# Kernel tuning notes

Hardware: AMD Instinct MI355X
Metric: run time of the kernel (lower is better)

Reference implementation:

```python
import jax, jax.numpy as jnp
import numpy as np

B, D, O = 256, 4096, 16384


def setup_inputs() -> dict:
    key = jax.random.key(0)
    k1, k2, k3, k4 = jax.random.split(key, 4)
    x1 = jax.random.normal(k1, (B, D), dtype=jnp.float32)
    x2 = jax.random.normal(k2, (B, D), dtype=jnp.float32)
    # random hash buckets in [0, O) and random +/-1 signs (homogeneous: shared by both inputs)
    h1 = jax.random.randint(k3, (D,), 0, O, dtype=jnp.int32)
    s1 = jnp.where(jax.random.uniform(k4, (D,)) < 0.5, -1.0, 1.0).astype(jnp.float32)
    return {"x1": x1, "x2": x2, "h1": h1, "s1": s1, "output_size": O}


def reference(x1, x2, h1, s1, output_size):
    # psi(): count-sketch via sign-multiply + scatter-add along feature axis
    batch = x1.shape[0]
    y1 = jnp.zeros((batch, output_size), x1.dtype).at[:, h1].add(s1 * x1)  # [B, O]
    y2 = jnp.zeros((batch, output_size), x2.dtype).at[:, h1].add(s1 * x2)  # [B, O]
    # conv(): circular convolution of the two sketches via FFT pointwise product
    out = jnp.fft.ifft(jnp.fft.fft(y1, axis=-1) * jnp.fft.fft(y2, axis=-1), axis=-1)
    return out.real.astype(x1.dtype)
```

## Files before the change

### kernel.cpp

```cpp
#include <hip/hip_runtime.h>


typedef float v2 __attribute__((ext_vector_type(2)));

#define N1      8192
#define BLOCK   1024
#define DIM     4096
#define PI_F    3.14159265358979323846f
#define RS2     0.70710678118654752f
#define SLOT(e) ((e) ^ (((e) >> 4) & 15))
#define REV13(x) ((int)(__brev((unsigned)(x)) >> 19))
#define WAVE_FENCE() __asm__ volatile("s_waitcnt lgkmcnt(0)" ::: "memory")

static __device__ __forceinline__ v2 cmul(v2 a, v2 b) {
    return a.xx * b + (v2){-a.y, a.y} * b.yx;
}
static __device__ __forceinline__ v2 csqr(v2 a) { return cmul(a, a); }
static __device__ __forceinline__ v2 expi(float phi) {
    float s, c; __sincosf(phi, &s, &c); return (v2){c, s};
}

static __device__ __forceinline__ void fft8_dif(v2* r, float phi) {
    v2 W2 = expi(phi), W1 = csqr(W2), W0 = csqr(W1);
    v2 W[3] = {W0, W1, W2};
    #pragma unroll
    for (int p = 2; p >= 0; --p) {
        #pragma unroll
        for (int h = 0; h < 4; ++h) {
            const int jp = h & ((1 << p) - 1);
            const int j  = ((h >> p) << (p + 1)) | jp;
            const int ci = jp << (2 - p);
            v2 Wp = W[p], T;
            if (ci == 0)      T = Wp;
            else if (ci == 2) T = (v2){Wp.y, -Wp.x};
            else if (ci == 1) T = cmul(Wp, (v2){RS2, -RS2});
            else              T = cmul(Wp, (v2){-RS2, -RS2});
            v2 a = r[j], bb = r[j + (1 << p)];
            r[j] = a + bb;
            r[j + (1 << p)] = cmul(a - bb, T);
        }
    }
}

static __device__ __forceinline__ void fft8_dit(v2* r, float phi) {
    v2 W2 = expi(phi), W1 = csqr(W2), W0 = csqr(W1);
    v2 W[3] = {W0, W1, W2};
    #pragma unroll
    for (int p = 0; p <= 2; ++p) {
        #pragma unroll
        for (int h = 0; h < 4; ++h) {
            const int jp = h & ((1 << p) - 1);
            const int j  = ((h >> p) << (p + 1)) | jp;
            const int ci = jp << (2 - p);
            v2 Wp = W[p], T;
            if (ci == 0)      T = Wp;
            else if (ci == 2) T = (v2){-Wp.y, Wp.x};
            else if (ci == 1) T = cmul(Wp, (v2){RS2, RS2});
            else              T = cmul(Wp, (v2){-RS2, RS2});
            v2 a = r[j], bb = cmul(r[j + (1 << p)], T);
            r[j]            = a + bb;
            r[j + (1 << p)] = a - bb;
        }
    }
}

static __device__ __forceinline__ void fft8_dit0(v2* r) {
    #pragma unroll
    for (int p = 0; p <= 2; ++p) {
        #pragma unroll
        for (int h = 0; h < 4; ++h) {
            const int jp = h & ((1 << p) - 1);
            const int j  = ((h >> p) << (p + 1)) | jp;
            const int ci = jp << (2 - p);
            v2 x = r[j + (1 << p)], bb;
            if (ci == 0)      bb = x;
            else if (ci == 2) bb = (v2){-x.y, x.x};
            else if (ci == 1) bb = cmul(x, (v2){RS2, RS2});
            else              bb = cmul(x, (v2){-RS2, RS2});
            v2 a = r[j];
            r[j] = a + bb; r[j + (1 << p)] = a - bb;
        }
    }
}

static __device__ __forceinline__ void fft4_difW4(v2& r0, v2& r1, v2& r2, v2& r3, v2 W1) {
    v2 W0 = csqr(W1);
    v2 a, bb;
    a = r0; bb = r2; r0 = a + bb; r2 = cmul(a - bb, W1);
    a = r1; bb = r3; r1 = a + bb;
    { v2 d = a - bb; r3 = cmul(d, (v2){W1.y, -W1.x}); }
    a = r0; bb = r1; r0 = a + bb; r1 = cmul(a - bb, W0);
    a = r2; bb = r3; r2 = a + bb; r3 = cmul(a - bb, W0);
}
static __device__ __forceinline__ void fft4_dif04(v2& r0, v2& r1, v2& r2, v2& r3) {
    v2 a, bb;
    a = r0; bb = r2; r0 = a + bb; r2 = a - bb;
    a = r1; bb = r3; r1 = a + bb;
    { v2 d = a - bb; r3 = (v2){d.y, -d.x}; }
    a = r0; bb = r1; r0 = a + bb; r1 = a - bb;
    a = r2; bb = r3; r2 = a + bb; r3 = a - bb;
}

static __device__ __forceinline__ void pair_slot(v2* zz, int j) {
    const int k  = REV13(j);
    const int kp = (N1 - k) & (N1 - 1);
    const int j2 = REV13(kp);
    v2 A = zz[SLOT(j)], B = zz[SLOT(j2)];
    v2 C = zz[N1 + SLOT(j)], D = zz[N1 + SLOT(j2)];
    v2 E  = (v2){0.5f * (A.x + B.x),  0.5f * (A.y - B.y)};
    v2 O  = (v2){0.5f * (A.y + B.y), -0.5f * (A.x - B.x)};
    v2 F  = (v2){0.5f * (C.x + D.x),  0.5f * (C.y - D.y)};
    v2 Ov = (v2){0.5f * (C.y + D.y), -0.5f * (C.x - D.x)};
    v2 Tm = expi(-PI_F * (float)k * (1.f / 8192.f));
    v2 u = cmul(Tm, O), v = cmul(Tm, Ov);
    v2 G = cmul(E + u, F + v);
    v2 H = cmul(E - u, F - v);
    v2 S  = (v2){0.5f * (G.x + H.x), 0.5f * (G.y + H.y)};
    v2 gh = G - H;
    v2 t2 = cmul((v2){Tm.x, -Tm.y}, gh);
    v2 Dv = (v2){-0.5f * t2.y, 0.5f * t2.x};
    zz[SLOT(j)]  = S + Dv;
    zz[SLOT(j2)] = (v2){S.x - Dv.x, -(S.y - Dv.y)};
}

__launch_bounds__(BLOCK, 4)
__global__ void cbp_fft_kernel(const float* __restrict__ x1,
                               const float* __restrict__ x2,
                               const int* __restrict__ h1,
                               const float* __restrict__ s1,
                               float* __restrict__ out) {
    __shared__ v2 zz[2 * N1];
    const int tid = threadIdx.x;
    const int l   = tid & 63;
    const int b   = blockIdx.x;
    float* zf = (float*)zz;

    const float* x1r = x1 + (size_t)b * DIM;
    const float* x2r = x2 + (size_t)b * DIM;
    float sv[DIM / BLOCK], a1[DIM / BLOCK], a2[DIM / BLOCK];
    int   hv[DIM / BLOCK];
    #pragma unroll
    for (int i = 0; i < DIM / BLOCK; ++i) {
        int d = tid + (i << 10);
        sv[i] = s1[d];
        hv[i] = h1[d];
        a1[i] = x1r[d];
        a2[i] = x2r[d];
    }

    {
        float4* z4 = (float4*)zz;
        #pragma unroll
        for (int j = 0; j < 8; ++j) z4[tid + (j << 10)] = make_float4(0.f, 0.f, 0.f, 0.f);
    }
    __syncthreads();

    #pragma unroll
    for (int i = 0; i < DIM / BLOCK; ++i) {
        int  h  = hv[i];
        int  fi = (SLOT(h >> 1) << 1) | (h & 1);
        atomicAdd(&zf[fi], sv[i] * a1[i]);
        atomicAdd(&zf[2 * N1 + fi], sv[i] * a2[i]);
    }
    __syncthreads();

    const int half = tid >> 9;
    const int tt   = tid & 511;
    const int hw   = tt >> 6;
    v2* Ah = zz + half * N1;

    #pragma unroll 1
    for (int q = 0; q < 2; ++q) {
        int k  = tt + (q << 9);
        int bs = k ^ ((k >> 4) & 15);
        v2 r[8];
        #pragma unroll
        for (int j = 0; j < 8; ++j) r[j] = Ah[bs + (j << 10)];
        fft8_dif(r, (float)k * (-PI_F / 4096.f));
        #pragma unroll
        for (int j = 0; j < 8; ++j) Ah[bs + (j << 10)] = r[j];
    }
    __syncthreads();

    #pragma unroll 1
    for (int q = 0; q < 2; ++q) {
        int kk = (tt & 63) + (q << 6);
        int bE = ((hw << 10) + kk) ^ (kk >> 4);
        int bO = bE ^ 8;
        v2 r[8];
        #pragma unroll
        for (int j = 0; j < 8; ++j) r[j] = Ah[((j & 1) ? bO : bE) + (j << 7)];
        fft8_dif(r, (float)kk * (-PI_F / 512.f));
        #pragma unroll
        for (int j = 0; j < 8; ++j) Ah[((j & 1) ? bO : bE) + (j << 7)] = r[j];
    }
    WAVE_FENCE();

    #pragma unroll 1
    for (int q = 0; q < 2; ++q) {
        int g  = (hw << 3) + ((l >> 4) << 1) + q;
        int kf = l & 15;
        int a0 = (g << 7) + (kf ^ (q << 3));
        v2 r[8];
        #pragma unroll
        for (int j = 0; j < 8; ++j) r[j] = Ah[(a0 ^ j) + (j << 4)];
        fft8_dif(r, (float)kf * (-PI_F / 64.f));
        #pragma unroll
        for (int j = 0; j < 8; ++j) Ah[(a0 ^ j) + (j << 4)] = r[j];
    }
    WAVE_FENCE();

    {
        const int span  = (hw << 6) + (l & 15) + ((l >> 4) << 4);
        const int sbase = (span << 4) + (span & 15);
        v2 R[16];
        #pragma unroll
        for (int m = 0; m < 16; ++m) R[m] = Ah[sbase ^ m];
        #pragma unroll
        for (int k4 = 0; k4 < 4; ++k4) {
            float c = (k4 & 1) ? ((k4 & 2) ? 0.38268343f : 0.92387953f)
                               : ((k4 & 2) ? 0.70710678f : 1.f);
            float s = (k4 & 1) ? ((k4 & 2) ? -0.92387953f : -0.38268343f)
                               : ((k4 & 2) ? -0.70710678f : 0.f);
            fft4_difW4(R[k4], R[k4 + 4], R[k4 + 8], R[k4 + 12], (v2){c, s});
        }
        #pragma unroll
        for (int q = 0; q < 4; ++q)
            fft4_dif04(R[4 * q], R[4 * q + 1], R[4 * q + 2], R[4 * q + 3]);
        #pragma unroll
        for (int m = 0; m < 16; ++m) Ah[sbase ^ m] = R[m];
    }
    __syncthreads();

    #pragma unroll 2
    for (int i = 0; i < 4; ++i) pair_slot(zz, (tid + (i << 10)) << 1);
    if (tid == 0) pair_slot(zz, 1);
    __syncthreads();

    {
        int B1 = (tid << 3) ^ ((tid >> 1) & 15);
        v2 r[8];
        #pragma unroll
        for (int i = 0; i < 8; ++i) r[i] = zz[B1 ^ i];
        fft8_dit0(r);
        #pragma unroll
        for (int i = 0; i < 8; ++i) zz[B1 ^ i] = r[i];
    }
    WAVE_FENCE();
    {
        int g = tid >> 3, k = tid & 7;
        int base = (g << 6) + k;
        v2 r[8];
        #pragma unroll
        for (int j = 0; j < 8; ++j) r[j] = zz[SLOT(base + (j << 3))];
        fft8_dit(r, (float)k * (PI_F / 32.f));
        #pragma unroll
        for (int j = 0; j < 8; ++j) zz[SLOT(base + (j << 3))] = r[j];
    }
    WAVE_FENCE();
    {
        int k = tid & 63;
        int base0 = ((tid >> 6) << 9) + (k & ~15);
        int Kh = k >> 4, K15 = k & 15;
        int B0  = base0 + (K15 ^ Kh);
        int Bm1 = base0 + (K15 ^ (Kh + 4));
        int Bm2 = base0 + (K15 ^ (Kh + 8));
        int Bm3 = base0 + (K15 ^ (Kh + 12));
        v2 r[8];
        r[0] = zz[B0];        r[1] = zz[Bm1 + 64];
        r[2] = zz[Bm2 + 128]; r[3] = zz[Bm3 + 192];
        r[4] = zz[B0 + 256];  r[5] = zz[Bm1 + 320];
        r[6] = zz[Bm2 + 384]; r[7] = zz[Bm3 + 448];
        fft8_dit(r, (float)k * (PI_F / 256.f));
        zz[B0]        = r[0]; zz[Bm1 + 64]  = r[1];
        zz[Bm2 + 128] = r[2]; zz[Bm3 + 192] = r[3];
        zz[B0 + 256]  = r[4]; zz[Bm1 + 320] = r[5];
        zz[Bm2 + 384] = r[6]; zz[Bm3 + 448] = r[7];
    }
    __syncthreads();
    {
        int g = tid >> 9, k = tid & 511;
        int bp = ((g << 12) + k) ^ ((k >> 4) & 15);
        v2 r[8];
        #pragma unroll
        for (int j = 0; j < 8; ++j) r[j] = zz[bp + (j << 9)];
        fft8_dit(r, (float)k * (PI_F / 2048.f));
        #pragma unroll
        for (int j = 0; j < 8; ++j) zz[bp + (j << 9)] = r[j];
    }
    __syncthreads();

    {
        float* outr = out + (size_t)b * (2 * N1);
        const float inv_n1 = 1.0f / (float)N1;
        const int b5 = (tid << 2) ^ ((tid >> 2) & 15);
        v2 Tn = expi(PI_F * (float)(tid << 2) * (1.f / 4096.f));
        const v2 STEP = (v2){0.99999970586288f, 7.6699031874270e-4f};
        v2 lo[4], hi[4];
        #pragma unroll
        for (int d5 = 0; d5 < 4; ++d5) {
            v2 a  = zz[b5 ^ d5];
            v2 bb = zz[(b5 ^ d5) + 4096];
            v2 tb = cmul(Tn, bb);
            lo[d5] = a + tb;
            hi[d5] = a - tb;
            if (d5 < 3) Tn = cmul(Tn, STEP);
        }
        float4 vlo0 = make_float4(lo[0].x * inv_n1, lo[0].y * inv_n1,
                                  lo[1].x * inv_n1, lo[1].y * inv_n1);
        float4 vlo1 = make_float4(lo[2].x * inv_n1, lo[2].y * inv_n1,
                                  lo[3].x * inv_n1, lo[3].y * inv_n1);
        float4 vhi0 = make_float4(hi[0].x * inv_n1, hi[0].y * inv_n1,
                                  hi[1].x * inv_n1, hi[1].y * inv_n1);
        float4 vhi1 = make_float4(hi[2].x * inv_n1, hi[2].y * inv_n1,
                                  hi[3].x * inv_n1, hi[3].y * inv_n1);
        *(float4*)(outr + (tid << 3))          = vlo0;
        *(float4*)(outr + (tid << 3) + 4)      = vlo1;
        *(float4*)(outr + N1 + (tid << 3))     = vhi0;
        *(float4*)(outr + N1 + (tid << 3) + 4) = vhi1;
    }
}

extern "C" void kernel_launch(void* const* d_in, const int* in_sizes, int n_in,
                              void* d_out, int out_size, void* d_ws, size_t ws_size,
                              hipStream_t stream) {
    const float* x1 = (const float*)d_in[0];
    const float* x2 = (const float*)d_in[1];
    const int*   h1 = (const int*)d_in[2];
    const float* s1 = (const float*)d_in[3];
    float* out = (float*)d_out;
    const int B = in_sizes[0] / DIM;
    cbp_fft_kernel<<<B, BLOCK, 0, stream>>>(x1, x2, h1, s1, out);
}
```

Baseline: 92.10 us.

## Replace four radix-8 inverse FFT passes with three radix-16 passes

```diff
diff --git a/kernel.cpp b/kernel.cpp
--- a/kernel.cpp
+++ b/kernel.cpp
@@ -8,6 +8,8 @@
 #define DIM     4096
 #define PI_F    3.14159265358979323846f
 #define RS2     0.70710678118654752f
+#define C8      0.92387953251128675f
+#define S8      0.38268343236508977f
 #define SLOT(e) ((e) ^ (((e) >> 4) & 15))
 #define REV13(x) ((int)(__brev((unsigned)(x)) >> 19))
 #define WAVE_FENCE() __asm__ volatile("s_waitcnt lgkmcnt(0)" ::: "memory")
@@ -42,21 +44,25 @@
     }
 }
 
-static __device__ __forceinline__ void fft8_dit(v2* r, float phi) {
-    v2 W2 = expi(phi), W1 = csqr(W2), W0 = csqr(W1);
-    v2 W[3] = {W0, W1, W2};
-    #pragma unroll
-    for (int p = 0; p <= 2; ++p) {
-        #pragma unroll
-        for (int h = 0; h < 4; ++h) {
+static __device__ __forceinline__ void fft16_dit(v2* r, float phi) {
+    v2 W3 = expi(phi), W2 = csqr(W3), W1 = csqr(W2), W0 = csqr(W1);
+    v2 W[4] = {W0, W1, W2, W3};
+    #pragma unroll
+    for (int p = 0; p <= 3; ++p) {
+        #pragma unroll
+        for (int h = 0; h < 8; ++h) {
             const int jp = h & ((1 << p) - 1);
             const int j  = ((h >> p) << (p + 1)) | jp;
-            const int ci = jp << (2 - p);
+            const int ci = jp << (3 - p);
             v2 Wp = W[p], T;
             if (ci == 0)      T = Wp;
-            else if (ci == 2) T = (v2){-Wp.y, Wp.x};
-            else if (ci == 1) T = cmul(Wp, (v2){RS2, RS2});
-            else              T = cmul(Wp, (v2){-RS2, RS2});
+            else if (ci == 4) T = (v2){-Wp.y, Wp.x};
+            else if (ci == 2) T = cmul(Wp, (v2){RS2, RS2});
+            else if (ci == 6) T = cmul(Wp, (v2){-RS2, RS2});
+            else if (ci == 1) T = cmul(Wp, (v2){C8, S8});
+            else if (ci == 3) T = cmul(Wp, (v2){S8, C8});
+            else if (ci == 5) T = cmul(Wp, (v2){-S8, C8});
+            else              T = cmul(Wp, (v2){-C8, S8});
             v2 a = r[j], bb = cmul(r[j + (1 << p)], T);
             r[j]            = a + bb;
             r[j + (1 << p)] = a - bb;
@@ -64,19 +70,23 @@
     }
 }
 
-static __device__ __forceinline__ void fft8_dit0(v2* r) {
-    #pragma unroll
-    for (int p = 0; p <= 2; ++p) {
-        #pragma unroll
-        for (int h = 0; h < 4; ++h) {
+static __device__ __forceinline__ void fft16_dit0(v2* r) {
+    #pragma unroll
+    for (int p = 0; p <= 3; ++p) {
+        #pragma unroll
+        for (int h = 0; h < 8; ++h) {
             const int jp = h & ((1 << p) - 1);
             const int j  = ((h >> p) << (p + 1)) | jp;
-            const int ci = jp << (2 - p);
+            const int ci = jp << (3 - p);
             v2 x = r[j + (1 << p)], bb;
             if (ci == 0)      bb = x;
-            else if (ci == 2) bb = (v2){-x.y, x.x};
-            else if (ci == 1) bb = cmul(x, (v2){RS2, RS2});
-            else              bb = cmul(x, (v2){-RS2, RS2});
+            else if (ci == 4) bb = (v2){-x.y, x.x};
+            else if (ci == 2) bb = cmul(x, (v2){RS2, RS2});
+            else if (ci == 6) bb = cmul(x, (v2){-RS2, RS2});
+            else if (ci == 1) bb = cmul(x, (v2){C8, S8});
+            else if (ci == 3) bb = cmul(x, (v2){S8, C8});
+            else if (ci == 5) bb = cmul(x, (v2){-S8, C8});
+            else              bb = cmul(x, (v2){-C8, S8});
             v2 a = r[j];
             r[j] = a + bb; r[j + (1 << p)] = a - bb;
         }
@@ -237,56 +247,38 @@
     if (tid == 0) pair_slot(zz, 1);
     __syncthreads();
 
-    {
-        int B1 = (tid << 3) ^ ((tid >> 1) & 15);
-        v2 r[8];
-        #pragma unroll
-        for (int i = 0; i < 8; ++i) r[i] = zz[B1 ^ i];
-        fft8_dit0(r);
-        #pragma unroll
-        for (int i = 0; i < 8; ++i) zz[B1 ^ i] = r[i];
+    if (tid < 512) {
+        const int Sb = (tid << 4) + (tid & 15);
+        v2 r[16];
+        #pragma unroll
+        for (int i = 0; i < 16; ++i) r[i] = zz[Sb ^ i];
+        fft16_dit0(r);
+        #pragma unroll
+        for (int i = 0; i < 16; ++i) zz[Sb ^ i] = r[i];
     }
     WAVE_FENCE();
-    {
-        int g = tid >> 3, k = tid & 7;
-        int base = (g << 6) + k;
-        v2 r[8];
-        #pragma unroll
-        for (int j = 0; j < 8; ++j) r[j] = zz[SLOT(base + (j << 3))];
-        fft8_dit(r, (float)k * (PI_F / 32.f));
-        #pragma unroll
-        for (int j = 0; j < 8; ++j) zz[SLOT(base + (j << 3))] = r[j];
-    }
-    WAVE_FENCE();
-    {
-        int k = tid & 63;
-        int base0 = ((tid >> 6) << 9) + (k & ~15);
-        int Kh = k >> 4, K15 = k & 15;
-        int B0  = base0 + (K15 ^ Kh);
-        int Bm1 = base0 + (K15 ^ (Kh + 4));
-        int Bm2 = base0 + (K15 ^ (Kh + 8));
-        int Bm3 = base0 + (K15 ^ (Kh + 12));
-        v2 r[8];
-        r[0] = zz[B0];        r[1] = zz[Bm1 + 64];
-        r[2] = zz[Bm2 + 128]; r[3] = zz[Bm3 + 192];
-        r[4] = zz[B0 + 256];  r[5] = zz[Bm1 + 320];
-        r[6] = zz[Bm2 + 384]; r[7] = zz[Bm3 + 448];
-        fft8_dit(r, (float)k * (PI_F / 256.f));
-        zz[B0]        = r[0]; zz[Bm1 + 64]  = r[1];
-        zz[Bm2 + 128] = r[2]; zz[Bm3 + 192] = r[3];
-        zz[B0 + 256]  = r[4]; zz[Bm1 + 320] = r[5];
-        zz[Bm2 + 384] = r[6]; zz[Bm3 + 448] = r[7];
-    }
-    __syncthreads();
-    {
-        int g = tid >> 9, k = tid & 511;
-        int bp = ((g << 12) + k) ^ ((k >> 4) & 15);
-        v2 r[8];
-        #pragma unroll
-        for (int j = 0; j < 8; ++j) r[j] = zz[bp + (j << 9)];
-        fft8_dit(r, (float)k * (PI_F / 2048.f));
-        #pragma unroll
-        for (int j = 0; j < 8; ++j) zz[bp + (j << 9)] = r[j];
+
+    if (tid < 512) {
+        const int g = tid >> 4, k = tid & 15;
+        const int Bz = g << 8;
+        v2 r[16];
+        #pragma unroll
+        for (int j = 0; j < 16; ++j) r[j] = zz[Bz + (j << 4) + (k ^ j)];
+        fft16_dit(r, (float)k * (PI_F / 128.f));
+        #pragma unroll
+        for (int j = 0; j < 16; ++j) zz[Bz + (j << 4) + (k ^ j)] = r[j];
+    }
+    __syncthreads();
+
+    if (tid < 512) {
+        const int g = tid >> 8, k = tid & 255;
+        const int C = (g << 12) + (k & 0xF0) + ((k & 15) ^ (k >> 4));
+        v2 r[16];
+        #pragma unroll
+        for (int j = 0; j < 16; ++j) r[j] = zz[C + (j << 8)];
+        fft16_dit(r, (float)k * (PI_F / 2048.f));
+        #pragma unroll
+        for (int j = 0; j < 16; ++j) zz[C + (j << 8)] = r[j];
     }
     __syncthreads();
 
```

New measurement: 92.70 us. No clear change (+0.7%).
